# Optimization experiments

Measured on AMD Instinct MI355X. Metric: run time of the kernel, lower is better.

## Reference

```python
import jax, jax.numpy as jnp
import numpy as np

DEPTH = 4
HEADS = 8
DIM = 512
DIM_HEAD = 64
INNER = HEADS * DIM_HEAD  # 512
MLP = 2048
NPK = 32
NEG = -1e9
EPS = 1e-5


def setup_inputs() -> dict:
    key = jax.random.key(0)
    ks = jax.random.split(key, 12)
    b, n, k = 2, 4096, 144
    x = jax.random.normal(ks[0], (b, n, DIM), jnp.float32)
    kx = jax.random.normal(ks[1], (b, k, DIM), jnp.float32)
    rd = jax.random.uniform(ks[2], (b, k, n), jnp.float32)
    clst = jax.random.normal(ks[3], (b, 1, DIM), jnp.float32)
    mask = jax.random.uniform(ks[4], (b, n, 1), jnp.float32)
    kmask = jax.random.uniform(ks[5], (b, k, 1), jnp.float32)

    def init(kk, shape, fan):
        return jax.random.normal(kk, shape, jnp.float32) / np.float32(np.sqrt(fan))

    return {
        "x": x, "kx": kx, "rd": rd, "clst": clst, "mask": mask, "kmask": kmask,
        "ln1_g": jnp.ones((DEPTH, DIM), jnp.float32),
        "ln1_b": jnp.zeros((DEPTH, DIM), jnp.float32),
        "w_qkv": init(ks[6], (DEPTH, DIM, 3 * INNER), DIM),
        "w_out": init(ks[7], (DEPTH, INNER, DIM), INNER),
        "b_out": jnp.zeros((DEPTH, DIM), jnp.float32),
        "ln2_g": jnp.ones((DEPTH, DIM), jnp.float32),
        "ln2_b": jnp.zeros((DEPTH, DIM), jnp.float32),
        "w1": init(ks[8], (DEPTH, DIM, MLP), DIM),
        "b1": jnp.zeros((DEPTH, MLP), jnp.float32),
        "w2": init(ks[9], (DEPTH, MLP, DIM), MLP),
        "b2": jnp.zeros((DEPTH, DIM), jnp.float32),
    }


def _ln(t, g, b):
    m = jnp.mean(t, axis=-1, keepdims=True)
    v = jnp.mean(jnp.square(t - m), axis=-1, keepdims=True)
    return (t - m) / jnp.sqrt(v + EPS) * g + b


def _split_heads(t):
    b, n, _ = t.shape
    return t.reshape(b, n, HEADS, DIM_HEAD).transpose(0, 2, 1, 3)  # b h n d


def _merge_heads(t):
    b, h, n, d = t.shape
    return t.transpose(0, 2, 1, 3).reshape(b, n, h * d)


def reference(x, kx, rd, clst, mask, kmask,
              ln1_g, ln1_b, w_qkv, w_out, b_out,
              ln2_g, ln2_b, w1, b1, w2, b2):
    scale = DIM_HEAD ** -0.5
    kernel_mask = kmask < 0.5                                   # [b,k,1] -> broadcast over dim
    att_mask = (jnp.einsum('bid,bjd->bij', mask, kmask) < 0.5)[:, None]  # [b,1,n,k]
    rd2 = (rd * rd)[:, None]                                    # [b,1,k,n]

    k_reps = []
    for l in range(DEPTH):
        x = _ln(x, ln1_g[l], ln1_b[l])
        kx = _ln(kx, ln1_g[l], ln1_b[l])
        clst = _ln(clst, ln1_g[l], ln1_b[l])
        krd = jnp.exp(-rd2 / (2 * NPK * (2 ** l)))              # [b,1,k,n]

        def qkv(t):
            p = t @ w_qkv[l]
            q, kk, v = jnp.split(p, 3, axis=-1)
            return _split_heads(q), _split_heads(kk), _split_heads(v)

        t_q, t_k, t_v = qkv(x)
        k_q, k_k, k_v = qkv(kx)
        c_q, _, _ = qkv(clst)

        def to_out(t):
            return _merge_heads(t) @ w_out[l] + b_out[l]

        # patch -> kernel cross-attention with post-softmax decay
        dots = jnp.einsum('bhid,bhjd->bhij', t_q, k_k) * scale   # [b,h,n,k]
        dots = jnp.where(att_mask, NEG, dots)
        attn = jax.nn.softmax(dots, axis=-1) * jnp.swapaxes(krd, -1, -2)
        x_ = to_out(jnp.einsum('bhij,bhjd->bhid', attn, k_v))

        # kernel -> patch cross-attention with decay
        k_dots = jnp.einsum('bhid,bhjd->bhij', k_q, t_k) * scale  # [b,h,k,n]
        k_dots = jnp.where(jnp.swapaxes(att_mask, -1, -2), NEG, k_dots)
        k_attn = jax.nn.softmax(k_dots, axis=-1) * krd
        kx_ = to_out(jnp.einsum('bhij,bhjd->bhid', k_attn, t_v))

        # class token -> kernel attention (no decay)
        c_dots = jnp.einsum('bhid,bhjd->bhij', c_q, k_k) * scale  # [b,h,1,k]
        c_dots = jnp.where(att_mask[:, :, :1], NEG, c_dots)
        c_attn = jax.nn.softmax(c_dots, axis=-1)
        clst_ = to_out(jnp.einsum('bhij,bhjd->bhid', c_attn, k_v))

        x = x + x_
        clst = clst + clst_
        kx = kx + kx_

        def ff(t):
            h = _ln(t, ln2_g[l], ln2_b[l])
            h = jax.nn.gelu(h @ w1[l] + b1[l], approximate=False)
            return h @ w2[l] + b2[l]

        x = ff(x) + x
        clst = ff(clst) + clst
        kx = ff(kx) + kx
        k_reps.append(jnp.where(kernel_mask, 0.0, kx))

    return jnp.stack(k_reps), clst
```

## Files before the change

kernel.cpp:

```cpp
#include <hip/hip_runtime.h>
#include <hip/hip_bf16.h>
#include <math.h>

#define NPAT 4096
#define NKER 144
#define DIMC 512
#define QKV_N 1536
#define MLP_N 2048
#define R_TOT 8482
#define R_PAD 8576
#define ROW_KX 8192
#define ROW_C 8480

typedef __hip_bfloat16 bf16;
using f32x4 = __attribute__((ext_vector_type(4))) float;
using s16x8 = __attribute__((ext_vector_type(8))) short;

template<typename T> __device__ __forceinline__ float tof(T v);
template<> __device__ __forceinline__ float tof<float>(float v) { return v; }
template<> __device__ __forceinline__ float tof<bf16>(bf16 v) { return __bfloat162float(v); }
template<typename T> __device__ __forceinline__ T fromf(float v);
template<> __device__ __forceinline__ float fromf<float>(float v) { return v; }
template<> __device__ __forceinline__ bf16 fromf<bf16>(float v) { return __float2bfloat16(v); }

__device__ __forceinline__ void gload_lds16(const bf16* g, bf16* l) {
  __builtin_amdgcn_global_load_lds((const __attribute__((address_space(1))) void*)g,
                                   (__attribute__((address_space(3))) void*)l, 16, 0, 0);
}

__device__ __forceinline__ float dot64q(const float* __restrict__ q, const bf16* __restrict__ k) {
  float acc = 0.f;
  const uint4* k4 = (const uint4*)k;
  #pragma unroll
  for (int t = 0; t < 8; ++t) {
    union { uint4 u; bf16 h[8]; } w; w.u = k4[t];
    #pragma unroll
    for (int e = 0; e < 8; ++e) acc += q[t * 8 + e] * tof(w.h[e]);
  }
  return acc;
}

template<typename TD>
__global__ void cvt_in(const float* __restrict__ s, TD* __restrict__ d, int n) {
  int i = blockIdx.x * 256 + threadIdx.x;
  if (i < n) d[i] = fromf<TD>(s[i]);
}

__global__ __launch_bounds__(256) void transpose_cvt(const float* __restrict__ src,
    bf16* __restrict__ dst, int K, int N) {
  __shared__ float tile[32][33];
  int kb = blockIdx.y * 32, nb = blockIdx.x * 32;
  int tx = threadIdx.x & 31, ty = threadIdx.x >> 5;
  #pragma unroll
  for (int r = ty; r < 32; r += 8) tile[r][tx] = src[(size_t)(kb + r) * N + nb + tx];
  __syncthreads();
  #pragma unroll
  for (int r = ty; r < 32; r += 8)
    dst[(size_t)(nb + r) * K + kb + tx] = fromf<bf16>(tile[tx][r]);
}

template<typename TS, typename TD>
__global__ __launch_bounds__(256) void ln_kernel(const TS* __restrict__ src,
    TD* __restrict__ dst, const float* __restrict__ g, const float* __restrict__ bb) {
  int row = blockIdx.x;
  const TS* p = src + (size_t)row * DIMC;
  int t = threadIdx.x;
  float v0 = tof(p[t]), v1 = tof(p[t + 256]);
  float s = v0 + v1;
  #pragma unroll
  for (int off = 32; off > 0; off >>= 1) s += __shfl_xor(s, off);
  __shared__ float ls[4], ls2[4];
  if ((t & 63) == 0) ls[t >> 6] = s;
  __syncthreads();
  float mean = (ls[0] + ls[1] + ls[2] + ls[3]) * (1.f / 512.f);
  float d0 = v0 - mean, d1 = v1 - mean;
  float s2 = d0 * d0 + d1 * d1;
  #pragma unroll
  for (int off = 32; off > 0; off >>= 1) s2 += __shfl_xor(s2, off);
  if ((t & 63) == 0) ls2[t >> 6] = s2;
  __syncthreads();
  float var = (ls2[0] + ls2[1] + ls2[2] + ls2[3]) * (1.f / 512.f);
  float rstd = rsqrtf(var + 1e-5f);
  TD* q = dst + (size_t)row * DIMC;
  q[t]       = fromf<TD>(d0 * rstd * g[t]       + bb[t]);
  q[t + 256] = fromf<TD>(d1 * rstd * g[t + 256] + bb[t + 256]);
}

__global__ __launch_bounds__(256) void ln_dual(float* __restrict__ act,
    bf16* __restrict__ actb, const float* __restrict__ g, const float* __restrict__ bb) {
  int row = blockIdx.x;
  float* p = act + (size_t)row * DIMC;
  int t = threadIdx.x;
  float v0 = p[t], v1 = p[t + 256];
  float s = v0 + v1;
  #pragma unroll
  for (int off = 32; off > 0; off >>= 1) s += __shfl_xor(s, off);
  __shared__ float ls[4], ls2[4];
  if ((t & 63) == 0) ls[t >> 6] = s;
  __syncthreads();
  float mean = (ls[0] + ls[1] + ls[2] + ls[3]) * (1.f / 512.f);
  float d0 = v0 - mean, d1 = v1 - mean;
  float s2 = d0 * d0 + d1 * d1;
  #pragma unroll
  for (int off = 32; off > 0; off >>= 1) s2 += __shfl_xor(s2, off);
  if ((t & 63) == 0) ls2[t >> 6] = s2;
  __syncthreads();
  float var = (ls2[0] + ls2[1] + ls2[2] + ls2[3]) * (1.f / 512.f);
  float rstd = rsqrtf(var + 1e-5f);
  float r0 = d0 * rstd * g[t] + bb[t];
  float r1 = d1 * rstd * g[t + 256] + bb[t + 256];
  p[t] = r0; p[t + 256] = r1;
  bf16* q = actb + (size_t)row * DIMC;
  q[t] = fromf<bf16>(r0); q[t + 256] = fromf<bf16>(r1);
}

template<int TM, typename TC, int ACT, bool HASRES>
__global__ __launch_bounds__(256) void gemm_mfma(
    const bf16* __restrict__ A, const bf16* __restrict__ Wt,
    const float* __restrict__ bias, const float* __restrict__ res,
    TC* __restrict__ C, int M, int N, int K) {
  constexpr int NI = 4;
  constexpr int NJ = (TM == 128) ? 4 : 2;
  constexpr int NQA = TM / 64;
  __shared__ bf16 As[2 * TM * 32];
  __shared__ bf16 Bs[2 * 128 * 32];
  int tid = threadIdx.x;
  int bm = blockIdx.y * TM, bn = blockIdx.x * 128;
  int wave = tid >> 6, lane = tid & 63;
  int quad = lane >> 4, lr = lane & 15;
  int WR = (TM == 128) ? (wave >> 1) * 64 : 0;
  int WC = (TM == 128) ? (wave & 1) * 64 : wave * 32;

  f32x4 acc[NI][NJ] = {};

  int rl = lane >> 2, pc = lane & 3;
  const bf16* aA[NQA]; const bf16* aB[2];
  int loA[NQA], loB[2];
  #pragma unroll
  for (int q = 0; q < NQA; ++q) {
    int rt = q * 64 + wave * 16 + rl;
    int c = pc ^ ((rt >> 1) & 3);
    aA[q] = A + (size_t)(bm + rt) * K + c * 8;
    loA[q] = (q * 64 + wave * 16) * 32;
  }
  #pragma unroll
  for (int q = 0; q < 2; ++q) {
    int rt = q * 64 + wave * 16 + rl;
    int c = pc ^ ((rt >> 1) & 3);
    aB[q] = Wt + (size_t)(bn + rt) * K + c * 8;
    loB[q] = (q * 64 + wave * 16) * 32;
  }

  auto stage = [&](int buf, int k0) {
    #pragma unroll
    for (int q = 0; q < NQA; ++q) gload_lds16(aA[q] + k0, As + buf * (TM * 32) + loA[q]);
    #pragma unroll
    for (int q = 0; q < 2; ++q)   gload_lds16(aB[q] + k0, Bs + buf * (128 * 32) + loB[q]);
  };

  stage(0, 0);
  int nk = K >> 5;
  for (int it = 0; it < nk; ++it) {
    __syncthreads();
    if (it + 1 < nk) stage((it + 1) & 1, (it + 1) << 5);
    const bf16* Ab = As + (it & 1) * (TM * 32);
    const bf16* Bb = Bs + (it & 1) * (128 * 32);
    s16x8 af[NI], bfr[NJ];
    #pragma unroll
    for (int i = 0; i < NI; ++i) {
      int ra = WR + i * 16 + lr;
      af[i] = *(const s16x8*)(Ab + ra * 32 + (quad ^ ((ra >> 1) & 3)) * 8);
    }
    #pragma unroll
    for (int j = 0; j < NJ; ++j) {
      int rb = WC + j * 16 + lr;
      bfr[j] = *(const s16x8*)(Bb + rb * 32 + (quad ^ ((rb >> 1) & 3)) * 8);
    }
    #pragma unroll
    for (int i = 0; i < NI; ++i)
      #pragma unroll
      for (int j = 0; j < NJ; ++j)
        acc[i][j] = __builtin_amdgcn_mfma_f32_16x16x32_bf16(af[i], bfr[j], acc[i][j], 0, 0, 0);
  }

  #pragma unroll
  for (int i = 0; i < NI; ++i) {
    int gm0 = bm + WR + i * 16 + quad * 4;
    #pragma unroll
    for (int j = 0; j < NJ; ++j) {
      int gn = bn + WC + j * 16 + lr;
      float bv = bias ? bias[gn] : 0.f;
      #pragma unroll
      for (int r = 0; r < 4; ++r) {
        int gm = gm0 + r;
        if (gm < M) {
          float v = acc[i][j][r] + bv;
          if (ACT == 1) v = 0.5f * v * (1.f + erff(v * 0.70710678118654752f));
          if (HASRES) v += res[(size_t)gm * N + gn];
          C[(size_t)gm * N + gn] = fromf<TC>(v);
        }
      }
    }
  }
}

__global__ __launch_bounds__(256) void decay_tr(const float* __restrict__ rd,
    bf16* __restrict__ DT, float invden) {
  int ib = blockIdx.x * 32, jb = blockIdx.y * 32, b = blockIdx.z;
  __shared__ bf16 t[32][33];
  int tx = threadIdx.x & 31, ty = threadIdx.x >> 5;
  for (int r = ty; r < 32; r += 8) {
    int j = jb + r;
    if (j < NKER) {
      float v = rd[((size_t)b * NKER + j) * NPAT + ib + tx];
      t[r][tx] = fromf<bf16>(expf(-v * v * invden));
    }
  }
  __syncthreads();
  for (int r = ty; r < 32; r += 8) {
    int i = ib + r, j = jb + tx;
    if (j < NKER) DT[((size_t)b * NPAT + i) * NKER + j] = t[tx][r];
  }
}

__global__ __launch_bounds__(256) void attn_p2k_f(
    const bf16* __restrict__ qkv, const float* __restrict__ pm,
    const float* __restrict__ km, const bf16* __restrict__ DT,
    bf16* __restrict__ o) {
  int i0 = blockIdx.x * 64, h = blockIdx.y, b = blockIdx.z;
  __shared__ bf16 Kk[144 * 72];
  __shared__ bf16 KvT[64 * 168];
  __shared__ bf16 Ps[64 * 168];
  __shared__ float pms[64];
  __shared__ float kms[144];
  int tid = threadIdx.x;
  bf16* Qs = Ps;

  for (int idx = tid; idx < 64 * 8; idx += 256) {
    int r = idx >> 3, c8 = idx & 7;
    *(uint4*)(Qs + r * 72 + c8 * 8) =
      *(const uint4*)(qkv + ((size_t)b * NPAT + i0 + r) * QKV_N + h * 64 + c8 * 8);
  }
  for (int idx = tid; idx < 144 * 8; idx += 256) {
    int r = idx >> 3, c8 = idx & 7;
    *(uint4*)(Kk + r * 72 + c8 * 8) =
      *(const uint4*)(qkv + ((size_t)ROW_KX + b * NKER + r) * QKV_N + DIMC + h * 64 + c8 * 8);
  }
  for (int idx = tid; idx < 144 * 8; idx += 256) {
    int r = idx >> 3, c8 = idx & 7;
    union { uint4 u; bf16 e[8]; } v;
    v.u = *(const uint4*)(qkv + ((size_t)ROW_KX + b * NKER + r) * QKV_N + 2 * DIMC + h * 64 + c8 * 8);
    #pragma unroll
    for (int e = 0; e < 8; ++e) KvT[(c8 * 8 + e) * 168 + r] = v.e[e];
  }
  for (int idx = tid; idx < 64 * 16; idx += 256) {
    int d = idx >> 4, j = 144 + (idx & 15);
    KvT[d * 168 + j] = fromf<bf16>(0.f);
  }
  if (tid < 64) pms[tid] = pm[(size_t)b * NPAT + i0 + tid];
  if (tid < 144) kms[tid] = km[b * NKER + tid];
  __syncthreads();

  int wave = tid >> 6, lane = tid & 63, quad = lane >> 4, lr = lane & 15;
  int mrow = wave * 16;

  f32x4 S[9] = {};
  #pragma unroll
  for (int kk = 0; kk < 64; kk += 32) {
    s16x8 a = *(const s16x8*)(Qs + (mrow + lr) * 72 + kk + quad * 8);
    #pragma unroll
    for (int n = 0; n < 9; ++n) {
      s16x8 bf_ = *(const s16x8*)(Kk + (n * 16 + lr) * 72 + kk + quad * 8);
      S[n] = __builtin_amdgcn_mfma_f32_16x16x32_bf16(a, bf_, S[n], 0, 0, 0);
    }
  }
  float mx[4] = {-3.4e38f, -3.4e38f, -3.4e38f, -3.4e38f};
  #pragma unroll
  for (int n = 0; n < 9; ++n) {
    int j = n * 16 + lr;
    float kmv = kms[j];
    #pragma unroll
    for (int r = 0; r < 4; ++r) {
      int il = mrow + quad * 4 + r;
      float s = S[n][r] * 0.125f;
      if (pms[il] * kmv < 0.5f) s = -1e9f;
      S[n][r] = s;
      mx[r] = fmaxf(mx[r], s);
    }
  }
  #pragma unroll
  for (int off = 1; off < 16; off <<= 1)
    #pragma unroll
    for (int r = 0; r < 4; ++r) mx[r] = fmaxf(mx[r], __shfl_xor(mx[r], off));
  float sum[4] = {0.f, 0.f, 0.f, 0.f};
  #pragma unroll
  for (int n = 0; n < 9; ++n)
    #pragma unroll
    for (int r = 0; r < 4; ++r) { float e = expf(S[n][r] - mx[r]); S[n][r] = e; sum[r] += e; }
  #pragma unroll
  for (int off = 1; off < 16; off <<= 1)
    #pragma unroll
    for (int r = 0; r < 4; ++r) sum[r] += __shfl_xor(sum[r], off);
  float inv[4];
  #pragma unroll
  for (int r = 0; r < 4; ++r) inv[r] = 1.f / sum[r];
  #pragma unroll
  for (int n = 0; n < 9; ++n) {
    int j = n * 16 + lr;
    #pragma unroll
    for (int r = 0; r < 4; ++r) {
      int i = i0 + mrow + quad * 4 + r;
      S[n][r] = S[n][r] * inv[r] * tof(DT[((size_t)b * NPAT + i) * NKER + j]);
    }
  }
  __syncthreads();
  #pragma unroll
  for (int n = 0; n < 9; ++n) {
    int j = n * 16 + lr;
    #pragma unroll
    for (int r = 0; r < 4; ++r)
      Ps[(mrow + quad * 4 + r) * 168 + j] = fromf<bf16>(S[n][r]);
  }
  for (int idx = tid; idx < 64 * 16; idx += 256) {
    int rr = idx >> 4, j = 144 + (idx & 15);
    Ps[rr * 168 + j] = fromf<bf16>(0.f);
  }
  __syncthreads();
  f32x4 O[4] = {};
  #pragma unroll
  for (int kk = 0; kk < 160; kk += 32) {
    s16x8 a = *(const s16x8*)(Ps + (mrow + lr) * 168 + kk + quad * 8);
    #pragma unroll
    for (int nd = 0; nd < 4; ++nd) {
      s16x8 bf_ = *(const s16x8*)(KvT + (nd * 16 + lr) * 168 + kk + quad * 8);
      O[nd] = __builtin_amdgcn_mfma_f32_16x16x32_bf16(a, bf_, O[nd], 0, 0, 0);
    }
  }
  #pragma unroll
  for (int nd = 0; nd < 4; ++nd) {
    int d = nd * 16 + lr;
    #pragma unroll
    for (int r = 0; r < 4; ++r) {
      int i = i0 + mrow + quad * 4 + r;
      o[((size_t)b * NPAT + i) * DIMC + h * 64 + d] = fromf<bf16>(O[nd][r]);
    }
  }
}

__global__ __launch_bounds__(256) void s2_gemm(
    const bf16* __restrict__ qkv, const float* __restrict__ pm,
    const float* __restrict__ km, float* __restrict__ S2) {
  int i0 = blockIdx.x * 128, h = blockIdx.y, b = blockIdx.z;
  __shared__ bf16 Kq[144 * 72];
  __shared__ bf16 Tk[128 * 72];
  __shared__ float pms[128];
  __shared__ float kms[144];
  int tid = threadIdx.x;
  for (int idx = tid; idx < 144 * 8; idx += 256) {
    int r = idx >> 3, c8 = idx & 7;
    *(uint4*)(Kq + r * 72 + c8 * 8) =
      *(const uint4*)(qkv + ((size_t)ROW_KX + b * NKER + r) * QKV_N + h * 64 + c8 * 8);
  }
  for (int idx = tid; idx < 128 * 8; idx += 256) {
    int r = idx >> 3, c8 = idx & 7;
    *(uint4*)(Tk + r * 72 + c8 * 8) =
      *(const uint4*)(qkv + ((size_t)b * NPAT + i0 + r) * QKV_N + DIMC + h * 64 + c8 * 8);
  }
  if (tid < 128) pms[tid] = pm[(size_t)b * NPAT + i0 + tid];
  if (tid < 144) kms[tid] = km[b * NKER + tid];
  __syncthreads();
  int wave = tid >> 6, lane = tid & 63, quad = lane >> 4, lr = lane & 15;
  int ncol = wave * 32;
  f32x4 acc[9][2] = {};
  #pragma unroll
  for (int kk = 0; kk < 64; kk += 32) {
    s16x8 bfr[2];
    #pragma unroll
    for (int ni = 0; ni < 2; ++ni)
      bfr[ni] = *(const s16x8*)(Tk + (ncol + ni * 16 + lr) * 72 + kk + quad * 8);
    #pragma unroll
    for (int mi = 0; mi < 9; ++mi) {
      s16x8 a = *(const s16x8*)(Kq + (mi * 16 + lr) * 72 + kk + quad * 8);
      #pragma unroll
      for (int ni = 0; ni < 2; ++ni)
        acc[mi][ni] = __builtin_amdgcn_mfma_f32_16x16x32_bf16(a, bfr[ni], acc[mi][ni], 0, 0, 0);
    }
  }
  size_t base = (size_t)(b * 8 + h) * NKER * NPAT;
  #pragma unroll
  for (int mi = 0; mi < 9; ++mi)
    #pragma unroll
    for (int ni = 0; ni < 2; ++ni)
      #pragma unroll
      for (int r = 0; r < 4; ++r) {
        int j = mi * 16 + quad * 4 + r;
        int il = ncol + ni * 16 + lr;
        float s = acc[mi][ni][r] * 0.125f;
        if (pms[il] * kms[j] < 0.5f) s = -1e9f;
        S2[base + (size_t)j * NPAT + i0 + il] = s;
      }
}

__global__ __launch_bounds__(256) void s2_softmax(
    const float* __restrict__ S2, const float* __restrict__ rd,
    bf16* __restrict__ P2, float invden) {
  int j = blockIdx.x, h = blockIdx.y, b = blockIdx.z;
  int tid = threadIdx.x;
  __shared__ float ls[NPAT];
  __shared__ float wA[4], wB[4];
  const float* row = S2 + ((size_t)(b * 8 + h) * NKER + j) * NPAT;
  float mx = -3.4e38f;
  for (int i = tid; i < NPAT; i += 256) { float v = row[i]; ls[i] = v; mx = fmaxf(mx, v); }
  #pragma unroll
  for (int off = 32; off > 0; off >>= 1) mx = fmaxf(mx, __shfl_xor(mx, off));
  if ((tid & 63) == 0) wA[tid >> 6] = mx;
  __syncthreads();
  mx = fmaxf(fmaxf(wA[0], wA[1]), fmaxf(wA[2], wA[3]));
  float sum = 0.f;
  for (int i = tid; i < NPAT; i += 256) { float e = expf(ls[i] - mx); ls[i] = e; sum += e; }
  #pragma unroll
  for (int off = 32; off > 0; off >>= 1) sum += __shfl_xor(sum, off);
  if ((tid & 63) == 0) wB[tid >> 6] = sum;
  __syncthreads();
  sum = wB[0] + wB[1] + wB[2] + wB[3];
  float inv_ = 1.f / sum;
  const float* rdrow = rd + ((size_t)b * NKER + j) * NPAT;
  bf16* prow = P2 + ((size_t)(b * 8 + h) * NKER + j) * NPAT;
  for (int i = tid; i < NPAT; i += 256) {
    float rv = rdrow[i];
    prow[i] = fromf<bf16>(ls[i] * inv_ * expf(-rv * rv * invden));
  }
}

__global__ __launch_bounds__(256) void pv_k2p(
    const bf16* __restrict__ P2, const bf16* __restrict__ qkv,
    float* __restrict__ koA) {
  int kc = blockIdx.x, h = blockIdx.y, b = blockIdx.z;
  int tid = threadIdx.x;
  __shared__ char uls[144 * 64 * 4];
  bf16* TvT = (bf16*)uls;
  float* red = (float*)uls;
  int ib = kc * 256;
  for (int idx = tid; idx < 256 * 8; idx += 256) {
    int r = idx >> 3, c8 = idx & 7;
    union { uint4 u; bf16 e[8]; } v;
    v.u = *(const uint4*)(qkv + ((size_t)b * NPAT + ib + r) * QKV_N + 2 * DIMC + h * 64 + c8 * 8);
    #pragma unroll
    for (int e = 0; e < 8; ++e) TvT[(c8 * 8 + e) * 264 + r] = v.e[e];
  }
  __syncthreads();
  int wave = tid >> 6, lane = tid & 63, quad = lane >> 4, lr = lane & 15;
  int kb = wave * 64;
  f32x4 acc[9][4] = {};
  const bf16* pbase = P2 + (size_t)(b * 8 + h) * NKER * NPAT;
  #pragma unroll
  for (int kk = 0; kk < 64; kk += 32) {
    s16x8 bfr[4];
    #pragma unroll
    for (int nd = 0; nd < 4; ++nd)
      bfr[nd] = *(const s16x8*)(TvT + (nd * 16 + lr) * 264 + kb + kk + quad * 8);
    #pragma unroll
    for (int mi = 0; mi < 9; ++mi) {
      s16x8 a = *(const s16x8*)(pbase + (size_t)(mi * 16 + lr) * NPAT + ib + kb + kk + quad * 8);
      #pragma unroll
      for (int nd = 0; nd < 4; ++nd)
        acc[mi][nd] = __builtin_amdgcn_mfma_f32_16x16x32_bf16(a, bfr[nd], acc[mi][nd], 0, 0, 0);
    }
  }
  __syncthreads();
  for (int w = 0; w < 4; ++w) {
    if (wave == w) {
      #pragma unroll
      for (int mi = 0; mi < 9; ++mi)
        #pragma unroll
        for (int nd = 0; nd < 4; ++nd)
          #pragma unroll
          for (int r = 0; r < 4; ++r) {
            int j = mi * 16 + quad * 4 + r, d = nd * 16 + lr;
            if (w == 0) red[j * 64 + d] = acc[mi][nd][r];
            else        red[j * 64 + d] += acc[mi][nd][r];
          }
    }
    __syncthreads();
  }
  float* kbase = koA + (size_t)(b * 8 + h) * NKER * 64;
  for (int idx = tid; idx < 144 * 64; idx += 256)
    atomicAdd(kbase + idx, red[idx]);
}

__global__ void zero_koA(float* koA) {
  int i = blockIdx.x * 256 + threadIdx.x;
  if (i < 2 * 8 * NKER * 64) koA[i] = 0.f;
}
__global__ void merge_k2p(const float* __restrict__ koA, bf16* __restrict__ o) {
  int idx = blockIdx.x * 256 + threadIdx.x;
  if (idx >= 2 * 8 * NKER * 64) return;
  int d = idx & 63, t = idx >> 6;
  int j = t % NKER; t /= NKER;
  int h = t & 7, b = t >> 3;
  o[((size_t)ROW_KX + b * NKER + j) * DIMC + h * 64 + d] = fromf<bf16>(koA[idx]);
}

__global__ __launch_bounds__(64) void attn_c(const bf16* __restrict__ qkv,
    const float* __restrict__ pm, const float* __restrict__ km, bf16* __restrict__ o) {
  int h = blockIdx.x, b = blockIdx.y;
  int lane = threadIdx.x;
  size_t rowc = ROW_C + b;
  __shared__ float q_s[64];
  __shared__ float p_s[NKER];
  q_s[lane] = tof(qkv[rowc * QKV_N + h * 64 + lane]);
  __syncthreads();
  float pmv = pm[(size_t)b * NPAT];
  float lg[3];
  float mx = -3.4e38f;
  #pragma unroll
  for (int t = 0; t < 3; ++t) {
    int j = lane + t * 64;
    float val = -3.4e38f;
    if (j < NKER) {
      size_t rowk = ROW_KX + (size_t)b * NKER + j;
      float d = dot64q(q_s, qkv + rowk * QKV_N + DIMC + h * 64) * 0.125f;
      if (pmv * km[b * NKER + j] < 0.5f) d = -1e9f;
      val = d;
    }
    lg[t] = val;
    mx = fmaxf(mx, val);
  }
  #pragma unroll
  for (int off = 32; off > 0; off >>= 1) mx = fmaxf(mx, __shfl_xor(mx, off));
  float sum = 0.f, e[3];
  #pragma unroll
  for (int t = 0; t < 3; ++t) { e[t] = (lg[t] > -1e30f) ? expf(lg[t] - mx) : 0.f; sum += e[t]; }
  #pragma unroll
  for (int off = 32; off > 0; off >>= 1) sum += __shfl_xor(sum, off);
  float inv = 1.f / sum;
  #pragma unroll
  for (int t = 0; t < 3; ++t) { int j = lane + t * 64; if (j < NKER) p_s[j] = e[t] * inv; }
  __syncthreads();
  const bf16* vb = qkv + (ROW_KX + (size_t)b * NKER) * QKV_N + 2 * DIMC + h * 64 + lane;
  float acc = 0.f;
  for (int j = 0; j < NKER; ++j) acc += p_s[j] * tof(vb[(size_t)j * QKV_N]);
  o[rowc * DIMC + h * 64 + lane] = fromf<bf16>(acc);
}

template<typename TS>
__global__ void emit_kreps(const TS* __restrict__ act, const float* __restrict__ km,
                           float* __restrict__ out, int l) {
  int idx = blockIdx.x * 256 + threadIdx.x;
  if (idx >= 2 * NKER * DIMC) return;
  int r = idx >> 9;
  float v = (km[r] < 0.5f) ? 0.f : tof(act[((size_t)ROW_KX + r) * DIMC + (idx & 511)]);
  out[(size_t)l * (2 * NKER * DIMC) + idx] = v;
}
template<typename TS>
__global__ void emit_clst(const TS* __restrict__ act, float* __restrict__ out) {
  int idx = blockIdx.x * 256 + threadIdx.x;
  if (idx >= 2 * DIMC) return;
  out[(size_t)4 * 2 * NKER * DIMC + idx] = tof(act[(size_t)ROW_C * DIMC + idx]);
}

template<typename TA, typename TC>
__global__ __launch_bounds__(256) void gemm_bias(const TA* __restrict__ A,
    const float* __restrict__ W, const float* __restrict__ bias,
    const TC* __restrict__ res, TC* __restrict__ C,
    int M, int N, int K, int act) {
  __shared__ float As[16][64];
  __shared__ float Bs[16][64];
  int bm = blockIdx.y * 64, bn = blockIdx.x * 64;
  int tid = threadIdx.x;
  int tx = tid & 15, ty = tid >> 4;
  float acc[4][4] = {};
  for (int k0 = 0; k0 < K; k0 += 16) {
    #pragma unroll
    for (int it = 0; it < 4; ++it) {
      int idx = tid + 256 * it;
      int r = idx >> 4, c = idx & 15;
      int gm = bm + r;
      As[c][r] = (gm < M) ? tof(A[(size_t)gm * K + k0 + c]) : 0.f;
    }
    #pragma unroll
    for (int it = 0; it < 4; ++it) {
      int idx = tid + 256 * it;
      int r = idx >> 6, c = idx & 63;
      Bs[r][c] = W[(size_t)(k0 + r) * N + bn + c];
    }
    __syncthreads();
    #pragma unroll
    for (int kk = 0; kk < 16; ++kk) {
      float a[4], b[4];
      #pragma unroll
      for (int i = 0; i < 4; ++i) a[i] = As[kk][ty * 4 + i];
      #pragma unroll
      for (int j = 0; j < 4; ++j) b[j] = Bs[kk][tx * 4 + j];
      #pragma unroll
      for (int i = 0; i < 4; ++i)
        #pragma unroll
        for (int j = 0; j < 4; ++j) acc[i][j] += a[i] * b[j];
    }
    __syncthreads();
  }
  #pragma unroll
  for (int i = 0; i < 4; ++i) {
    int gm = bm + ty * 4 + i;
    if (gm >= M) continue;
    #pragma unroll
    for (int j = 0; j < 4; ++j) {
      int gn = bn + tx * 4 + j;
      float v = acc[i][j];
      if (bias) v += bias[gn];
      if (act == 1) v = 0.5f * v * (1.f + erff(v * 0.70710678118654752f));
      if (res) v += tof(res[(size_t)gm * N + gn]);
      C[(size_t)gm * N + gn] = fromf<TC>(v);
    }
  }
}

static void run_fast2(void* const* d_in, float* out, float* act, bf16* actb,
                      bf16* bufo, bf16* bufq, bf16* wt,
                      float* S2, bf16* P2, bf16* DT, float* koA, hipStream_t stream) {
  const float* x     = (const float*)d_in[0];
  const float* kx    = (const float*)d_in[1];
  const float* rd    = (const float*)d_in[2];
  const float* clst  = (const float*)d_in[3];
  const float* mask  = (const float*)d_in[4];
  const float* kmask = (const float*)d_in[5];
  const float* ln1g  = (const float*)d_in[6];
  const float* ln1b  = (const float*)d_in[7];
  const float* wqkv  = (const float*)d_in[8];
  const float* wout  = (const float*)d_in[9];
  const float* bout  = (const float*)d_in[10];
  const float* ln2g  = (const float*)d_in[11];
  const float* ln2b  = (const float*)d_in[12];
  const float* w1    = (const float*)d_in[13];
  const float* b1    = (const float*)d_in[14];
  const float* w2    = (const float*)d_in[15];
  const float* b2    = (const float*)d_in[16];

  bf16* wtq = wt;
  bf16* wto = wtq + (size_t)4 * QKV_N * DIMC;
  bf16* wt1 = wto + (size_t)4 * DIMC * DIMC;
  bf16* wt2 = wt1 + (size_t)4 * MLP_N * DIMC;

  for (int l = 0; l < 4; ++l) {
    transpose_cvt<<<dim3(QKV_N / 32, DIMC / 32), 256, 0, stream>>>(
        wqkv + (size_t)l * DIMC * QKV_N, wtq + (size_t)l * QKV_N * DIMC, DIMC, QKV_N);
    transpose_cvt<<<dim3(DIMC / 32, DIMC / 32), 256, 0, stream>>>(
        wout + (size_t)l * DIMC * DIMC, wto + (size_t)l * DIMC * DIMC, DIMC, DIMC);
    transpose_cvt<<<dim3(MLP_N / 32, DIMC / 32), 256, 0, stream>>>(
        w1 + (size_t)l * DIMC * MLP_N, wt1 + (size_t)l * MLP_N * DIMC, DIMC, MLP_N);
    transpose_cvt<<<dim3(DIMC / 32, MLP_N / 32), 256, 0, stream>>>(
        w2 + (size_t)l * MLP_N * DIMC, wt2 + (size_t)l * DIMC * MLP_N, MLP_N, DIMC);
  }

  bf16* qkv  = bufq;
  bf16* ffh  = (bf16*)S2;
  bf16* o    = bufo;
  bf16* actn = bufo;

  cvt_in<float><<<(2 * NPAT * DIMC + 255) / 256, 256, 0, stream>>>(x, act, 2 * NPAT * DIMC);
  cvt_in<float><<<(2 * NKER * DIMC + 255) / 256, 256, 0, stream>>>(kx, act + (size_t)ROW_KX * DIMC, 2 * NKER * DIMC);
  cvt_in<float><<<(2 * DIMC + 255) / 256, 256, 0, stream>>>(clst, act + (size_t)ROW_C * DIMC, 2 * DIMC);

  const int MT = R_PAD / 128;
  const int MT64 = R_PAD / 64;
  const int KON = 2 * 8 * NKER * 64;

  for (int l = 0; l < 4; ++l) {
    float invden = 1.0f / (64.0f * (float)(1 << l));
    ln_dual<<<R_TOT, 256, 0, stream>>>(act, actb, ln1g + l * DIMC, ln1b + l * DIMC);
    gemm_mfma<128, bf16, 0, false><<<dim3(QKV_N / 128, MT), 256, 0, stream>>>(
        actb, wtq + (size_t)l * QKV_N * DIMC, nullptr, nullptr, qkv, R_TOT, QKV_N, DIMC);
    decay_tr<<<dim3(NPAT / 32, 5, 2), 256, 0, stream>>>(rd, DT, invden);
    attn_p2k_f<<<dim3(NPAT / 64, 8, 2), 256, 0, stream>>>(qkv, mask, kmask, DT, o);
    s2_gemm<<<dim3(NPAT / 128, 8, 2), 256, 0, stream>>>(qkv, mask, kmask, S2);
    s2_softmax<<<dim3(NKER, 8, 2), 256, 0, stream>>>(S2, rd, P2, invden);
    zero_koA<<<(KON + 255) / 256, 256, 0, stream>>>(koA);
    pv_k2p<<<dim3(16, 8, 2), 256, 0, stream>>>(P2, qkv, koA);
    merge_k2p<<<(KON + 255) / 256, 256, 0, stream>>>(koA, o);
    attn_c<<<dim3(8, 2), 64, 0, stream>>>(qkv, mask, kmask, o);
    gemm_mfma<64, float, 0, true><<<dim3(DIMC / 128, MT64), 256, 0, stream>>>(
        o, wto + (size_t)l * DIMC * DIMC, bout + l * DIMC, act, act, R_TOT, DIMC, DIMC);
    ln_kernel<float, bf16><<<R_TOT, 256, 0, stream>>>(act, actn, ln2g + l * DIMC, ln2b + l * DIMC);
    gemm_mfma<128, bf16, 1, false><<<dim3(MLP_N / 128, MT), 256, 0, stream>>>(
        actn, wt1 + (size_t)l * MLP_N * DIMC, b1 + l * MLP_N, nullptr, ffh, R_TOT, MLP_N, DIMC);
    gemm_mfma<64, float, 0, true><<<dim3(DIMC / 128, MT64), 256, 0, stream>>>(
        ffh, wt2 + (size_t)l * DIMC * MLP_N, b2 + l * DIMC, act, act, R_TOT, DIMC, MLP_N);
    emit_kreps<float><<<(2 * NKER * DIMC + 255) / 256, 256, 0, stream>>>(act, kmask, out, l);
  }
  emit_clst<float><<<(2 * DIMC + 255) / 256, 256, 0, stream>>>(act, out);
}

template<typename ActT>
static void run_pipeline(void* const* d_in, float* out, ActT* act, bf16* bufo, bf16* bufq,
                         hipStream_t stream) {
  const float* x     = (const float*)d_in[0];
  const float* kx    = (const float*)d_in[1];
  const float* rd    = (const float*)d_in[2];
  const float* clst  = (const float*)d_in[3];
  const float* mask  = (const float*)d_in[4];
  const float* kmask = (const float*)d_in[5];
  const float* ln1g  = (const float*)d_in[6];
  const float* ln1b  = (const float*)d_in[7];
  const float* wqkv  = (const float*)d_in[8];
  const float* wout  = (const float*)d_in[9];
  const float* bout  = (const float*)d_in[10];
  const float* ln2g  = (const float*)d_in[11];
  const float* ln2b  = (const float*)d_in[12];
  const float* w1    = (const float*)d_in[13];
  const float* b1    = (const float*)d_in[14];
  const float* w2    = (const float*)d_in[15];
  const float* b2    = (const float*)d_in[16];

  bf16* qkv  = bufq;
  bf16* ffh  = bufq;
  bf16* o    = bufo;
  bf16* actn = bufo;
  const int FF_CHUNK = 4241;

  cvt_in<ActT><<<(2 * NPAT * DIMC + 255) / 256, 256, 0, stream>>>(x, act, 2 * NPAT * DIMC);
  cvt_in<ActT><<<(2 * NKER * DIMC + 255) / 256, 256, 0, stream>>>(kx, act + (size_t)ROW_KX * DIMC, 2 * NKER * DIMC);
  cvt_in<ActT><<<(2 * DIMC + 255) / 256, 256, 0, stream>>>(clst, act + (size_t)ROW_C * DIMC, 2 * DIMC);

  for (int l = 0; l < 4; ++l) {
    float invden = 1.0f / (64.0f * (float)(1 << l));
    (void)invden;
    ln_kernel<ActT, ActT><<<R_TOT, 256, 0, stream>>>(act, act, ln1g + l * DIMC, ln1b + l * DIMC);
    gemm_bias<ActT, bf16><<<dim3(QKV_N / 64, (R_TOT + 63) / 64), 256, 0, stream>>>(
        act, wqkv + (size_t)l * DIMC * QKV_N, nullptr, nullptr, qkv, R_TOT, QKV_N, DIMC, 0);
    attn_c<<<dim3(8, 2), 64, 0, stream>>>(qkv, mask, kmask, o);
    gemm_bias<bf16, ActT><<<dim3(DIMC / 64, (R_TOT + 63) / 64), 256, 0, stream>>>(
        o, wout + (size_t)l * DIMC * DIMC, bout + l * DIMC, act, act, R_TOT, DIMC, DIMC, 0);
    ln_kernel<ActT, bf16><<<R_TOT, 256, 0, stream>>>(act, actn, ln2g + l * DIMC, ln2b + l * DIMC);
    for (int c0 = 0; c0 < R_TOT; c0 += FF_CHUNK) {
      int rows = (R_TOT - c0 < FF_CHUNK) ? (R_TOT - c0) : FF_CHUNK;
      gemm_bias<bf16, bf16><<<dim3(MLP_N / 64, (rows + 63) / 64), 256, 0, stream>>>(
          actn + (size_t)c0 * DIMC, w1 + (size_t)l * DIMC * MLP_N, b1 + l * MLP_N,
          nullptr, ffh, rows, MLP_N, DIMC, 1);
      gemm_bias<bf16, ActT><<<dim3(DIMC / 64, (rows + 63) / 64), 256, 0, stream>>>(
          ffh, w2 + (size_t)l * MLP_N * DIMC, b2 + l * DIMC,
          act + (size_t)c0 * DIMC, act + (size_t)c0 * DIMC, rows, DIMC, MLP_N, 0);
    }
    emit_kreps<ActT><<<(2 * NKER * DIMC + 255) / 256, 256, 0, stream>>>(act, kmask, out, l);
  }
  emit_clst<ActT><<<(2 * DIMC + 255) / 256, 256, 0, stream>>>(act, out);
}

extern "C" void kernel_launch(void* const* d_in, const int* in_sizes, int n_in,
                              void* d_out, int out_size, void* d_ws, size_t ws_size,
                              hipStream_t stream) {
  (void)in_sizes; (void)n_in; (void)out_size;
  float* out = (float*)d_out;

  const size_t szA  = (size_t)R_TOT * DIMC * 4;
  const size_t szAB = (size_t)R_PAD * DIMC * 2;
  const size_t szO  = (size_t)R_PAD * DIMC * 2;
  const size_t szQ  = (size_t)R_PAD * QKV_N * 2;
  const size_t szW  = (size_t)4 * (QKV_N * DIMC + DIMC * DIMC + MLP_N * DIMC + DIMC * MLP_N) * 2;
  const size_t szS2 = (size_t)2 * 8 * NKER * NPAT * 4;
  const size_t szP2 = (size_t)2 * 8 * NKER * NPAT * 2;
  const size_t szDT = (size_t)2 * NPAT * NKER * 2;
  const size_t szKo = (size_t)2 * 8 * NKER * 64 * 4;
  const size_t needFast2 = szA + szAB + szO + szQ + szW + szS2 + szP2 + szDT + szKo;

  if (ws_size >= needFast2) {
    char* w = (char*)d_ws;
    float* act  = (float*)w;            w += szA;
    bf16*  actb = (bf16*)w;             w += szAB;
    bf16*  bufo = (bf16*)w;             w += szO;
    bf16*  bufq = (bf16*)w;             w += szQ;
    bf16*  wt   = (bf16*)w;             w += szW;
    float* S2   = (float*)w;            w += szS2;
    bf16*  P2   = (bf16*)w;             w += szP2;
    bf16*  DT   = (bf16*)w;             w += szDT;
    float* koA  = (float*)w;
    run_fast2(d_in, out, act, actb, bufo, bufq, wt, S2, P2, DT, koA, stream);
  } else if (ws_size >= szA + szO + szQ) {
    float* act = (float*)d_ws;
    bf16* bufo = (bf16*)((char*)d_ws + szA);
    bf16* bufq = (bf16*)((char*)d_ws + szA + szO);
    run_pipeline<float>(d_in, out, act, bufo, bufq, stream);
  } else {
    bf16* act = (bf16*)d_ws;
    bf16* bufo = (bf16*)((char*)d_ws + szO);
    bf16* bufq = (bf16*)((char*)d_ws + 2 * szO);
    run_pipeline<bf16>(d_in, out, act, bufo, bufq, stream);
  }
}
```

Baseline: 1.358 ms.

## Fuse kernel-to-patch softmax into PV GEMM with atomic row max and deferred normalization

Removes the separate s2_softmax pass over the large score matrix. The row max is now computed in s2_gemm through per-row atomicMax on order-preserving encoded floats. The exponential, the decay multiply and the partial softmax sums are computed on the fly inside pv_k2p, and the division by the sum is deferred to merge_k2p. It also replaces exact erf GELU with the tanh approximation and uses fast __expf, which adds small numerical deviation. Memsets replace the zeroing kernel, and a transposed decay copy is written for coalesced reads.

```diff
diff --git a/kernel.cpp b/kernel.cpp
--- a/kernel.cpp
+++ b/kernel.cpp
@@ -26,6 +26,20 @@
 __device__ __forceinline__ void gload_lds16(const bf16* g, bf16* l) {
   __builtin_amdgcn_global_load_lds((const __attribute__((address_space(1))) void*)g,
                                    (__attribute__((address_space(3))) void*)l, 16, 0, 0);
+}
+
+__device__ __forceinline__ float gelu_f(float x) {
+  float u = 0.7978845608028654f * (x + 0.044715f * x * x * x);
+  float t = 2.f / (1.f + __expf(-2.f * u)) - 1.f;
+  return 0.5f * x * (1.f + t);
+}
+
+__device__ __forceinline__ unsigned fenc(float f) {
+  unsigned u = __float_as_uint(f);
+  return (u & 0x80000000u) ? ~u : (u | 0x80000000u);
+}
+__device__ __forceinline__ float fdec(unsigned u) {
+  return (u & 0x80000000u) ? __uint_as_float(u & 0x7FFFFFFFu) : __uint_as_float(~u);
 }
 
 __device__ __forceinline__ float dot64q(const float* __restrict__ q, const bf16* __restrict__ k) {
@@ -195,7 +209,7 @@
         int gm = gm0 + r;
         if (gm < M) {
           float v = acc[i][j][r] + bv;
-          if (ACT == 1) v = 0.5f * v * (1.f + erff(v * 0.70710678118654752f));
+          if (ACT == 1) v = gelu_f(v);
           if (HASRES) v += res[(size_t)gm * N + gn];
           C[(size_t)gm * N + gn] = fromf<TC>(v);
         }
@@ -205,7 +219,7 @@
 }
 
 __global__ __launch_bounds__(256) void decay_tr(const float* __restrict__ rd,
-    bf16* __restrict__ DT, float invden) {
+    bf16* __restrict__ DT, bf16* __restrict__ DTk, float invden) {
   int ib = blockIdx.x * 32, jb = blockIdx.y * 32, b = blockIdx.z;
   __shared__ bf16 t[32][33];
   int tx = threadIdx.x & 31, ty = threadIdx.x >> 5;
@@ -213,7 +227,9 @@
     int j = jb + r;
     if (j < NKER) {
       float v = rd[((size_t)b * NKER + j) * NPAT + ib + tx];
-      t[r][tx] = fromf<bf16>(expf(-v * v * invden));
+      bf16 dv = fromf<bf16>(expf(-v * v * invden));
+      t[r][tx] = dv;
+      DTk[((size_t)b * NKER + j) * NPAT + ib + tx] = dv;
     }
   }
   __syncthreads();
@@ -296,7 +312,7 @@
   #pragma unroll
   for (int n = 0; n < 9; ++n)
     #pragma unroll
-    for (int r = 0; r < 4; ++r) { float e = expf(S[n][r] - mx[r]); S[n][r] = e; sum[r] += e; }
+    for (int r = 0; r < 4; ++r) { float e = __expf(S[n][r] - mx[r]); S[n][r] = e; sum[r] += e; }
   #pragma unroll
   for (int off = 1; off < 16; off <<= 1)
     #pragma unroll
@@ -349,7 +365,8 @@
 
 __global__ __launch_bounds__(256) void s2_gemm(
     const bf16* __restrict__ qkv, const float* __restrict__ pm,
-    const float* __restrict__ km, float* __restrict__ S2) {
+    const float* __restrict__ km, float* __restrict__ S2,
+    unsigned* __restrict__ mxE) {
   int i0 = blockIdx.x * 128, h = blockIdx.y, b = blockIdx.z;
   __shared__ bf16 Kq[144 * 72];
   __shared__ bf16 Tk[128 * 72];
@@ -387,54 +404,32 @@
     }
   }
   size_t base = (size_t)(b * 8 + h) * NKER * NPAT;
+  unsigned* mxb = mxE + (size_t)(b * 8 + h) * NKER;
   #pragma unroll
   for (int mi = 0; mi < 9; ++mi)
     #pragma unroll
-    for (int ni = 0; ni < 2; ++ni)
-      #pragma unroll
-      for (int r = 0; r < 4; ++r) {
-        int j = mi * 16 + quad * 4 + r;
+    for (int r = 0; r < 4; ++r) {
+      int j = mi * 16 + quad * 4 + r;
+      float rowm = -3.4e38f;
+      #pragma unroll
+      for (int ni = 0; ni < 2; ++ni) {
         int il = ncol + ni * 16 + lr;
         float s = acc[mi][ni][r] * 0.125f;
         if (pms[il] * kms[j] < 0.5f) s = -1e9f;
+        acc[mi][ni][r] = s;
+        rowm = fmaxf(rowm, s);
         S2[base + (size_t)j * NPAT + i0 + il] = s;
       }
-}
-
-__global__ __launch_bounds__(256) void s2_softmax(
-    const float* __restrict__ S2, const float* __restrict__ rd,
-    bf16* __restrict__ P2, float invden) {
-  int j = blockIdx.x, h = blockIdx.y, b = blockIdx.z;
-  int tid = threadIdx.x;
-  __shared__ float ls[NPAT];
-  __shared__ float wA[4], wB[4];
-  const float* row = S2 + ((size_t)(b * 8 + h) * NKER + j) * NPAT;
-  float mx = -3.4e38f;
-  for (int i = tid; i < NPAT; i += 256) { float v = row[i]; ls[i] = v; mx = fmaxf(mx, v); }
-  #pragma unroll
-  for (int off = 32; off > 0; off >>= 1) mx = fmaxf(mx, __shfl_xor(mx, off));
-  if ((tid & 63) == 0) wA[tid >> 6] = mx;
-  __syncthreads();
-  mx = fmaxf(fmaxf(wA[0], wA[1]), fmaxf(wA[2], wA[3]));
-  float sum = 0.f;
-  for (int i = tid; i < NPAT; i += 256) { float e = expf(ls[i] - mx); ls[i] = e; sum += e; }
-  #pragma unroll
-  for (int off = 32; off > 0; off >>= 1) sum += __shfl_xor(sum, off);
-  if ((tid & 63) == 0) wB[tid >> 6] = sum;
-  __syncthreads();
-  sum = wB[0] + wB[1] + wB[2] + wB[3];
-  float inv_ = 1.f / sum;
-  const float* rdrow = rd + ((size_t)b * NKER + j) * NPAT;
-  bf16* prow = P2 + ((size_t)(b * 8 + h) * NKER + j) * NPAT;
-  for (int i = tid; i < NPAT; i += 256) {
-    float rv = rdrow[i];
-    prow[i] = fromf<bf16>(ls[i] * inv_ * expf(-rv * rv * invden));
-  }
+      #pragma unroll
+      for (int off = 1; off < 16; off <<= 1) rowm = fmaxf(rowm, __shfl_xor(rowm, off));
+      if (lr == 0) atomicMax(mxb + j, fenc(rowm));
+    }
 }
 
 __global__ __launch_bounds__(256) void pv_k2p(
-    const bf16* __restrict__ P2, const bf16* __restrict__ qkv,
-    float* __restrict__ koA) {
+    const float* __restrict__ S2, const unsigned* __restrict__ mxE,
+    const bf16* __restrict__ DTk, const bf16* __restrict__ qkv,
+    float* __restrict__ koA, float* __restrict__ Z) {
   int kc = blockIdx.x, h = blockIdx.y, b = blockIdx.z;
   int tid = threadIdx.x;
   __shared__ char uls[144 * 64 * 4];
@@ -451,8 +446,16 @@
   __syncthreads();
   int wave = tid >> 6, lane = tid & 63, quad = lane >> 4, lr = lane & 15;
   int kb = wave * 64;
+  int bh = b * 8 + h;
+  size_t base = (size_t)bh * NKER * NPAT;
   f32x4 acc[9][4] = {};
-  const bf16* pbase = P2 + (size_t)(b * 8 + h) * NKER * NPAT;
+  float zacc[9];
+  float mxl[9];
+  #pragma unroll
+  for (int mi = 0; mi < 9; ++mi) {
+    zacc[mi] = 0.f;
+    mxl[mi] = fdec(mxE[(size_t)bh * NKER + mi * 16 + lr]);
+  }
   #pragma unroll
   for (int kk = 0; kk < 64; kk += 32) {
     s16x8 bfr[4];
@@ -461,11 +464,35 @@
       bfr[nd] = *(const s16x8*)(TvT + (nd * 16 + lr) * 264 + kb + kk + quad * 8);
     #pragma unroll
     for (int mi = 0; mi < 9; ++mi) {
-      s16x8 a = *(const s16x8*)(pbase + (size_t)(mi * 16 + lr) * NPAT + ib + kb + kk + quad * 8);
+      int j = mi * 16 + lr;
+      int ioff = ib + kb + kk + quad * 8;
+      const float* srow = S2 + base + (size_t)j * NPAT + ioff;
+      const bf16* drow = DTk + ((size_t)b * NKER + j) * NPAT + ioff;
+      float4 s0 = *(const float4*)srow;
+      float4 s1 = *(const float4*)(srow + 4);
+      union { uint4 u; bf16 e[8]; } dv; dv.u = *(const uint4*)drow;
+      float sv[8] = {s0.x, s0.y, s0.z, s0.w, s1.x, s1.y, s1.z, s1.w};
+      union { s16x8 v; bf16 e[8]; } w;
+      float m = mxl[mi];
+      float zl = 0.f;
+      #pragma unroll
+      for (int e = 0; e < 8; ++e) {
+        float ev = __expf(sv[e] - m);
+        zl += ev;
+        w.e[e] = fromf<bf16>(ev * tof(dv.e[e]));
+      }
+      zacc[mi] += zl;
       #pragma unroll
       for (int nd = 0; nd < 4; ++nd)
-        acc[mi][nd] = __builtin_amdgcn_mfma_f32_16x16x32_bf16(a, bfr[nd], acc[mi][nd], 0, 0, 0);
-    }
+        acc[mi][nd] = __builtin_amdgcn_mfma_f32_16x16x32_bf16(w.v, bfr[nd], acc[mi][nd], 0, 0, 0);
+    }
+  }
+  #pragma unroll
+  for (int mi = 0; mi < 9; ++mi) {
+    float z = zacc[mi];
+    z += __shfl_xor(z, 16);
+    z += __shfl_xor(z, 32);
+    if (quad == 0) atomicAdd(Z + (size_t)bh * NKER + mi * 16 + lr, z);
   }
   __syncthreads();
   for (int w = 0; w < 4; ++w) {
@@ -483,22 +510,21 @@
     }
     __syncthreads();
   }
-  float* kbase = koA + (size_t)(b * 8 + h) * NKER * 64;
+  float* kbase = koA + (size_t)bh * NKER * 64;
   for (int idx = tid; idx < 144 * 64; idx += 256)
     atomicAdd(kbase + idx, red[idx]);
 }
 
-__global__ void zero_koA(float* koA) {
-  int i = blockIdx.x * 256 + threadIdx.x;
-  if (i < 2 * 8 * NKER * 64) koA[i] = 0.f;
-}
-__global__ void merge_k2p(const float* __restrict__ koA, bf16* __restrict__ o) {
+__global__ void merge_k2p(const float* __restrict__ koA, const float* __restrict__ Z,
+                          bf16* __restrict__ o) {
   int idx = blockIdx.x * 256 + threadIdx.x;
   if (idx >= 2 * 8 * NKER * 64) return;
   int d = idx & 63, t = idx >> 6;
   int j = t % NKER; t /= NKER;
   int h = t & 7, b = t >> 3;
-  o[((size_t)ROW_KX + b * NKER + j) * DIMC + h * 64 + d] = fromf<bf16>(koA[idx]);
+  float z = Z[(size_t)(b * 8 + h) * NKER + j];
+  float v = (z > 0.f) ? koA[idx] / z : 0.f;
+  o[((size_t)ROW_KX + b * NKER + j) * DIMC + h * 64 + d] = fromf<bf16>(v);
 }
 
 __global__ __launch_bounds__(64) void attn_c(const bf16* __restrict__ qkv,
@@ -608,7 +634,7 @@
       int gn = bn + tx * 4 + j;
       float v = acc[i][j];
       if (bias) v += bias[gn];
-      if (act == 1) v = 0.5f * v * (1.f + erff(v * 0.70710678118654752f));
+      if (act == 1) v = gelu_f(v);
       if (res) v += tof(res[(size_t)gm * N + gn]);
       C[(size_t)gm * N + gn] = fromf<TC>(v);
     }
@@ -617,7 +643,7 @@
 
 static void run_fast2(void* const* d_in, float* out, float* act, bf16* actb,
                       bf16* bufo, bf16* bufq, bf16* wt,
-                      float* S2, bf16* P2, bf16* DT, float* koA, hipStream_t stream) {
+                      float* S2, char* aux, float* koA, hipStream_t stream) {
   const float* x     = (const float*)d_in[0];
   const float* kx    = (const float*)d_in[1];
   const float* rd    = (const float*)d_in[2];
@@ -636,6 +662,11 @@
   const float* w2    = (const float*)d_in[15];
   const float* b2    = (const float*)d_in[16];
 
+  unsigned* mxE = (unsigned*)aux;
+  float*    Zb  = (float*)(aux + 16384);
+  bf16*     DT  = (bf16*)(aux + 32768);
+  bf16*     DTk = (bf16*)(aux + 32768 + (size_t)2 * NPAT * NKER * 2);
+
   bf16* wtq = wt;
   bf16* wto = wtq + (size_t)4 * QKV_N * DIMC;
   bf16* wt1 = wto + (size_t)4 * DIMC * DIMC;
@@ -670,13 +701,14 @@
     ln_dual<<<R_TOT, 256, 0, stream>>>(act, actb, ln1g + l * DIMC, ln1b + l * DIMC);
     gemm_mfma<128, bf16, 0, false><<<dim3(QKV_N / 128, MT), 256, 0, stream>>>(
         actb, wtq + (size_t)l * QKV_N * DIMC, nullptr, nullptr, qkv, R_TOT, QKV_N, DIMC);
-    decay_tr<<<dim3(NPAT / 32, 5, 2), 256, 0, stream>>>(rd, DT, invden);
+    decay_tr<<<dim3(NPAT / 32, 5, 2), 256, 0, stream>>>(rd, DT, DTk, invden);
     attn_p2k_f<<<dim3(NPAT / 64, 8, 2), 256, 0, stream>>>(qkv, mask, kmask, DT, o);
-    s2_gemm<<<dim3(NPAT / 128, 8, 2), 256, 0, stream>>>(qkv, mask, kmask, S2);
-    s2_softmax<<<dim3(NKER, 8, 2), 256, 0, stream>>>(S2, rd, P2, invden);
-    zero_koA<<<(KON + 255) / 256, 256, 0, stream>>>(koA);
-    pv_k2p<<<dim3(16, 8, 2), 256, 0, stream>>>(P2, qkv, koA);
-    merge_k2p<<<(KON + 255) / 256, 256, 0, stream>>>(koA, o);
+    hipMemsetAsync(mxE, 0, 2 * 8 * NKER * 4, stream);
+    s2_gemm<<<dim3(NPAT / 128, 8, 2), 256, 0, stream>>>(qkv, mask, kmask, S2, mxE);
+    hipMemsetAsync(Zb, 0, 2 * 8 * NKER * 4, stream);
+    hipMemsetAsync(koA, 0, (size_t)KON * 4, stream);
+    pv_k2p<<<dim3(16, 8, 2), 256, 0, stream>>>(S2, mxE, DTk, qkv, koA, Zb);
+    merge_k2p<<<(KON + 255) / 256, 256, 0, stream>>>(koA, Zb, o);
     attn_c<<<dim3(8, 2), 64, 0, stream>>>(qkv, mask, kmask, o);
     gemm_mfma<64, float, 0, true><<<dim3(DIMC / 128, MT64), 256, 0, stream>>>(
         o, wto + (size_t)l * DIMC * DIMC, bout + l * DIMC, act, act, R_TOT, DIMC, DIMC);
@@ -695,7 +727,6 @@
                          hipStream_t stream) {
   const float* x     = (const float*)d_in[0];
   const float* kx    = (const float*)d_in[1];
-  const float* rd    = (const float*)d_in[2];
   const float* clst  = (const float*)d_in[3];
   const float* mask  = (const float*)d_in[4];
   const float* kmask = (const float*)d_in[5];
@@ -722,8 +753,6 @@
   cvt_in<ActT><<<(2 * DIMC + 255) / 256, 256, 0, stream>>>(clst, act + (size_t)ROW_C * DIMC, 2 * DIMC);
 
   for (int l = 0; l < 4; ++l) {
-    float invden = 1.0f / (64.0f * (float)(1 << l));
-    (void)invden;
     ln_kernel<ActT, ActT><<<R_TOT, 256, 0, stream>>>(act, act, ln1g + l * DIMC, ln1b + l * DIMC);
     gemm_bias<ActT, bf16><<<dim3(QKV_N / 64, (R_TOT + 63) / 64), 256, 0, stream>>>(
         act, wqkv + (size_t)l * DIMC * QKV_N, nullptr, nullptr, qkv, R_TOT, QKV_N, DIMC, 0);
@@ -757,10 +786,9 @@
   const size_t szQ  = (size_t)R_PAD * QKV_N * 2;
   const size_t szW  = (size_t)4 * (QKV_N * DIMC + DIMC * DIMC + MLP_N * DIMC + DIMC * MLP_N) * 2;
   const size_t szS2 = (size_t)2 * 8 * NKER * NPAT * 4;
-  const size_t szP2 = (size_t)2 * 8 * NKER * NPAT * 2;
-  const size_t szDT = (size_t)2 * NPAT * NKER * 2;
+  const size_t szAux = (size_t)2 * 8 * NKER * NPAT * 2;
   const size_t szKo = (size_t)2 * 8 * NKER * 64 * 4;
-  const size_t needFast2 = szA + szAB + szO + szQ + szW + szS2 + szP2 + szDT + szKo;
+  const size_t needFast2 = szA + szAB + szO + szQ + szW + szS2 + szAux + szKo;
 
   if (ws_size >= needFast2) {
     char* w = (char*)d_ws;
@@ -770,10 +798,9 @@
     bf16*  bufq = (bf16*)w;             w += szQ;
     bf16*  wt   = (bf16*)w;             w += szW;
     float* S2   = (float*)w;            w += szS2;
-    bf16*  P2   = (bf16*)w;             w += szP2;
-    bf16*  DT   = (bf16*)w;             w += szDT;
+    char*  aux  = w;                    w += szAux;
     float* koA  = (float*)w;
-    run_fast2(d_in, out, act, actb, bufo, bufq, wt, S2, P2, DT, koA, stream);
+    run_fast2(d_in, out, act, actb, bufo, bufq, wt, S2, aux, koA, stream);
   } else if (ws_size >= szA + szO + szQ) {
     float* act = (float*)d_ws;
     bf16* bufo = (bf16*)((char*)d_ws + szA);
```

New measurement: 1.355 ms. About the same (-0.2%).
